# Kernel tuning notes

Measured on AMD Instinct MI355X. Metric: run time of the kernel, lower is better.

Reference implementation:

```python
import jax, jax.numpy as jnp
import numpy as np

D_MODEL = 768; HEADS = 8; LAYERS = 2

def pos_encoding(n, d):
    pos = np.arange(n, dtype=np.float32)[:, None]
    div = np.exp(np.arange(0, d, 2, dtype=np.float32) * -(np.log(10000.0) / d))
    pe = np.zeros((n, d), np.float32)
    pe[:, 0::2] = np.sin(pos * div)
    pe[:, 1::2] = np.cos(pos * div)
    return jnp.asarray(pe)

def layer_norm(x, g, b):
    m = x.mean(-1, keepdims=True)
    v = ((x - m) ** 2).mean(-1, keepdims=True)
    return (x - m) / jnp.sqrt(v + 1e-6) * g + b

def mha(k_in, v_in, q_in, mask, Wq, bq, Wk, bk, Wv, bv, Wout, bout):
    # BertSum MultiHeadedAttention(key, value, query, mask); mask True = blocked
    B, Lq, d = q_in.shape
    dk = d // HEADS
    def proj(x, W, b):
        y = x @ W + b
        return y.reshape(B, x.shape[1], HEADS, dk).transpose(0, 2, 1, 3)
    q = proj(q_in, Wq, bq)
    k = proj(k_in, Wk, bk)
    v = proj(v_in, Wv, bv)
    scores = jnp.einsum('bhqd,bhkd->bhqk', q, k) / jnp.sqrt(jnp.float32(dk))
    scores = jnp.where(mask[:, None, :, :], jnp.float32(-1e18), scores)
    attn = jax.nn.softmax(scores, axis=-1)
    out = jnp.einsum('bhqk,bhkd->bhqd', attn, v).transpose(0, 2, 1, 3).reshape(B, Lq, d)
    return out @ Wout + bout

def ffn(x, W1, b1, W2, b2, g, b):
    # PositionwiseFeedForward: x + w2(gelu(w1(LN(x))))
    return x + jax.nn.gelu(layer_norm(x, g, b) @ W1 + b1) @ W2 + b2

def setup_inputs():
    key = jax.random.key(0)
    ks = jax.random.split(key, 20)
    B, N_TOP, N_OUT, D, DFF, DH = 8, 512, 64, D_MODEL, 3072, 512
    s = 0.02
    return {
        'top_vecs': jax.random.normal(ks[0], (B, N_TOP, D), jnp.float32),
        'inputs': jax.random.normal(ks[1], (B, N_OUT, D), jnp.float32),
        'mask': jnp.ones((B, N_TOP), bool),
        'label_mask': jnp.ones((B, N_OUT), bool),
        'Wq': jax.random.normal(ks[2], (LAYERS, D, D)) * s,
        'bq': jnp.zeros((LAYERS, D)),
        'Wk': jax.random.normal(ks[3], (LAYERS, D, D)) * s,
        'bk': jnp.zeros((LAYERS, D)),
        'Wv': jax.random.normal(ks[4], (LAYERS, D, D)) * s,
        'bv': jnp.zeros((LAYERS, D)),
        'Wout': jax.random.normal(ks[5], (LAYERS, D, D)) * s,
        'bout': jnp.zeros((LAYERS, D)),
        'W1': jax.random.normal(ks[6], (LAYERS, D, DFF)) * s,
        'b1': jnp.zeros((LAYERS, DFF)),
        'W2': jax.random.normal(ks[7], (LAYERS, DFF, D)) * s,
        'b2': jnp.zeros((LAYERS, D)),
        'ln_g': jnp.ones((LAYERS, D)),
        'ln_b': jnp.zeros((LAYERS, D)),
        'Wo': jax.random.normal(ks[8], (D, DH)) * s,
        'bo': jnp.zeros((DH,)),
        'Wi': jax.random.normal(ks[9], (D, DH)) * s,
        'bi': jnp.zeros((DH,)),
        'v_w': jax.random.normal(ks[10], (DH,)) * s,
        'v_b': jnp.zeros(()),
    }

def reference(top_vecs, inputs, mask, label_mask, Wq, bq, Wk, bk, Wv, bv, Wout, bout,
              W1, b1, W2, b2, ln_g, ln_b, Wo, bo, Wi, bi, v_w, v_b):
    B, n_out, d = inputs.shape
    pe = pos_encoding(n_out, d)
    seq_mask = jnp.triu(jnp.ones((n_out, n_out), bool), 1)  # future positions blocked
    self_mask = (~label_mask)[:, None, :] | seq_mask[None]  # (B, n_out, n_out)
    ctx_mask = jnp.broadcast_to((~mask)[:, None, :], (B, n_out, mask.shape[1]))
    x = inputs + pe[None]
    for i in range(LAYERS):
        ctx = mha(x, x, x, self_mask, Wq[i], bq[i], Wk[i], bk[i], Wv[i], bv[i], Wout[i], bout[i])
        dec = mha(top_vecs, top_vecs, ctx, ctx_mask, Wq[i], bq[i], Wk[i], bk[i], Wv[i], bv[i], Wout[i], bout[i])
        x = ffn(dec, W1[i], b1[i], W2[i], b2[i], ln_g[i], ln_b[i])
    # additive-attention scoring head: (B, n_out, n_top, d_hidden) broadcast intermediate
    h = jax.nn.leaky_relu((x @ Wo + bo)[:, :, None, :] + (top_vecs @ Wi + bi)[:, None, :, :])
    scores = jnp.einsum('bonh,h->bon', h, v_w) + v_b
    return jax.nn.softmax(scores, axis=-1)
```

## Files before the change

### kernel.cpp

```cpp
#include <hip/hip_runtime.h>
#include <math.h>

#define D_MODEL 768
#define HEADS   8
#define DK      96
#define NB      8
#define N_TOP   512
#define N_OUT   64
#define DFF     3072
#define DH      512

typedef short  short8  __attribute__((ext_vector_type(8)));
typedef short  short4v __attribute__((ext_vector_type(4)));
typedef float  floatx4 __attribute__((ext_vector_type(4)));

__device__ __forceinline__ unsigned short f2bf(float f) {
    unsigned int u = __float_as_uint(f);
    u += 0x7fffu + ((u >> 16) & 1u);
    return (unsigned short)(u >> 16);
}
__device__ __forceinline__ float bf2f(unsigned short h) {
    return __uint_as_float(((unsigned int)h) << 16);
}

__device__ __forceinline__ float gelu_f(float x) {
    const float c = 0.7978845608028654f;
    return 0.5f * x * (1.0f + tanhf(c * (x + 0.044715f * x * x * x)));
}

__device__ __forceinline__ void gl16(const short* g, short* l) {
    __builtin_amdgcn_global_load_lds(
        (const __attribute__((address_space(1))) void*)g,
        (__attribute__((address_space(3))) void*)l, 16, 0, 0);
}

__device__ __forceinline__ float block_reduce_sum(float v, float* red) {
    int tid = threadIdx.x;
    red[tid] = v;
    __syncthreads();
    for (int s = blockDim.x >> 1; s > 0; s >>= 1) {
        if (tid < s) red[tid] += red[tid + s];
        __syncthreads();
    }
    float r = red[0];
    __syncthreads();
    return r;
}
__device__ __forceinline__ float block_reduce_max(float v, float* red) {
    int tid = threadIdx.x;
    red[tid] = v;
    __syncthreads();
    for (int s = blockDim.x >> 1; s > 0; s >>= 1) {
        if (tid < s) red[tid] = fmaxf(red[tid], red[tid + s]);
        __syncthreads();
    }
    float r = red[0];
    __syncthreads();
    return r;
}

struct TPack {
    const float* src[14];
    short*       dst[14];
    int K[14], N[14];
    int tstart[15];
};

__global__ __launch_bounds__(256) void multi_transpose_kernel(TPack pk) {
    __shared__ float t[32][33];
    int tile = blockIdx.x;
    int i = 0;
    while (i < 13 && tile >= pk.tstart[i + 1]) ++i;
    int lt = tile - pk.tstart[i];
    int K = pk.K[i], N = pk.N[i];
    int ntx = N >> 5;
    int bx = lt % ntx, by = lt / ntx;
    const float* in = pk.src[i];
    short* out = pk.dst[i];
    int tx = threadIdx.x & 31, ty = threadIdx.x >> 5;
#pragma unroll
    for (int r = 0; r < 4; ++r)
        t[ty + r * 8][tx] = in[(size_t)(by * 32 + ty + r * 8) * N + bx * 32 + tx];
    __syncthreads();
#pragma unroll
    for (int r = 0; r < 4; ++r)
        out[(size_t)(bx * 32 + ty + r * 8) * K + by * 32 + tx] =
            (short)f2bf(t[tx][ty + r * 8]);
}

__global__ void prep_kernel(const float* __restrict__ top, const float* __restrict__ inp,
                            short* __restrict__ top_bf, short* __restrict__ xb,
                            const short* __restrict__ WTq0, const short* __restrict__ WTq1,
                            const float* __restrict__ bout, const float* __restrict__ bq,
                            float* __restrict__ bqc,
                            int nkv4, int nx4) {
    int i = blockIdx.x * blockDim.x + threadIdx.x;
    if (i < nkv4) {
        float4 v = ((const float4*)top)[i];
        top_bf[i * 4 + 0] = (short)f2bf(v.x);
        top_bf[i * 4 + 1] = (short)f2bf(v.y);
        top_bf[i * 4 + 2] = (short)f2bf(v.z);
        top_bf[i * 4 + 3] = (short)f2bf(v.w);
        return;
    }
    int j = i - nkv4;
    if (j < nx4) {
#pragma unroll
        for (int u = 0; u < 4; ++u) {
            int idx = j * 4 + u;
            int c   = idx % D_MODEL;
            int pos = (idx / D_MODEL) % N_OUT;
            int jj  = c >> 1;
            float ang = (float)pos * expf((float)(2 * jj) * (-logf(10000.0f) / (float)D_MODEL));
            float pe  = (c & 1) ? cosf(ang) : sinf(ang);
            xb[idx] = (short)f2bf(inp[idx] + pe);
        }
        return;
    }
    int g = j - nx4;
    if (g >= 2 * D_MODEL) return;
    int L = g / D_MODEL, n = g % D_MODEL;
    const short* wr = (L == 0 ? WTq0 : WTq1) + (size_t)n * D_MODEL;
    const float* bo_ = bout + (size_t)L * D_MODEL;
    float s = bq[(size_t)L * D_MODEL + n];
    for (int k = 0; k < D_MODEL; k += 8) {
        short8 w = *(const short8*)(wr + k);
#pragma unroll
        for (int u = 0; u < 8; ++u)
            s += bo_[k + u] * bf2f((unsigned short)w[u]);
    }
    bqc[(size_t)L * D_MODEL + n] = s;
}

struct GDesc {
    const short* A;
    const short* Bt;
    int K;
    int nbx;
    short*       dst[3];
    const float* bias[3];
    int cum[4];
    int vtlog[3];
    int nseg;
};
struct GPack {
    GDesc d[5];
    int nd;
    int start[6];
};

__global__ __launch_bounds__(256) void gemm128g_kernel(GPack gp) {
    __shared__ __align__(16) short As[2 * 64 * 32];
    __shared__ __align__(16) short Bs[2 * 128 * 32];

    const int blk = blockIdx.x;
    int di = 0;
    while (di + 1 < gp.nd && blk >= gp.start[di + 1]) ++di;
    const GDesc& D = gp.d[di];
    const int l = blk - gp.start[di];
    const int bm = (l / D.nbx) * 64, bn = (l % D.nbx) * 128;
    const int K = D.K;
    const int nst = K >> 5;

    const int tid  = threadIdx.x;
    const int wave = tid >> 6, lane = tid & 63;
    const int wr = wave >> 1, wc = wave & 1;
    const int lc = lane & 15;
    const int lq = lane >> 4;
    const int lr4 = lq * 4;
    const int ko  = lq * 8;

    const int srA = wave * 16 + (lane >> 2);
    const int srB = wave * 32 + (lane >> 2);
    const int scol = (lane & 3) * 8;
    const int sbA = wave * 512;
    const int sbB = wave * 1024;

    floatx4 acc[2][4];
#pragma unroll
    for (int i = 0; i < 2; ++i)
#pragma unroll
        for (int j = 0; j < 4; ++j) acc[i][j] = (floatx4)0.0f;

    const short* Ab = D.A  + (size_t)(bm + srA) * K + scol;
    const short* Bb = D.Bt + (size_t)(bn + srB) * K + scol;
    const size_t hq = (size_t)16 * K;

#define STG(t, buf) do {                                          \
        gl16(Ab + (size_t)(t) * 32,      As + (buf) * 2048 + sbA);\
        gl16(Bb + (size_t)(t) * 32,      Bs + (buf) * 4096 + sbB);\
        gl16(Bb + (size_t)(t) * 32 + hq, Bs + (buf) * 4096 + sbB + 512);\
    } while (0)

    STG(0, 0);
    __syncthreads();

    int cur = 0;
    for (int t = 0; t < nst; ++t) {
        if (t + 1 < nst) STG(t + 1, cur ^ 1);
        const short* Ar = As + cur * 2048;
        const short* Br = Bs + cur * 4096;
        short8 a[2], b[4];
#pragma unroll
        for (int f = 0; f < 2; ++f)
            a[f] = *(const short8*)&Ar[(wr * 32 + f * 16 + lc) * 32 + ko];
#pragma unroll
        for (int f = 0; f < 4; ++f)
            b[f] = *(const short8*)&Br[(wc * 64 + f * 16 + lc) * 32 + ko];
#pragma unroll
        for (int fr = 0; fr < 2; ++fr)
#pragma unroll
            for (int fc = 0; fc < 4; ++fc)
                acc[fr][fc] = __builtin_amdgcn_mfma_f32_16x16x32_bf16(
                    a[fr], b[fc], acc[fr][fc], 0, 0, 0);
        __syncthreads();
        cur ^= 1;
    }
#undef STG

#pragma unroll
    for (int fc = 0; fc < 4; ++fc) {
        int col = bn + wc * 64 + fc * 16 + lc;
        int s = 0;
        while (s + 1 < D.nseg && col >= D.cum[s + 1]) ++s;
        int cl   = col - D.cum[s];
        int segw = D.cum[s + 1] - D.cum[s];
        const float* bp = D.bias[s];
        short* dst = D.dst[s];
        int vtl = D.vtlog[s];
        float bi = bp ? bp[cl] : 0.0f;
#pragma unroll
        for (int fr = 0; fr < 2; ++fr)
#pragma unroll
            for (int r = 0; r < 4; ++r) {
                int row = bm + wr * 32 + fr * 16 + lr4 + r;
                float x = acc[fr][fc][r] + bi;
                if (vtl) {
                    int seq = 1 << vtl;
                    dst[((size_t)(row >> vtl) * segw + cl) * seq + (row & (seq - 1))] =
                        (short)f2bf(x);
                } else {
                    dst[(size_t)row * segw + cl] = (short)f2bf(x);
                }
            }
    }
}

__global__ __launch_bounds__(256) void gemm_bf16_kernel(
    const short* __restrict__ A, const short* __restrict__ Bt,
    const float* __restrict__ bias0, const float* __restrict__ bias1,
    const float* __restrict__ bias2, const float* __restrict__ residual,
    float* __restrict__ Cf, short* __restrict__ Cb0, short* __restrict__ Cb1,
    short* __restrict__ Cb2, float* __restrict__ part,
    int M, int N, int K, int act, int segw, int vt_seg, int vt_log) {
    __shared__ __align__(16) short As[2 * 2 * 64 * 32];
    __shared__ __align__(16) short Bs[2 * 2 * 64 * 32];

    const int bm = blockIdx.y * 64, bn = blockIdx.x * 64;
    const int nz = gridDim.z, kz = blockIdx.z;
    const int kchunk = K / nz;

    const int tid  = threadIdx.x;
    const int wave = tid >> 6, lane = tid & 63;
    const int wr = wave >> 1, wc = wave & 1;
    const int lc = lane & 15;
    const int lr4 = (lane >> 4) * 4;
    const int ko  = (lane >> 4) * 8;

    const int srow = wave * 16 + (lane >> 2);
    const int scol = (lane & 3) * 8;
    const int sbase = wave * 512;

    const int nst = kchunk >> 6;

    floatx4 acc[2][2];
#pragma unroll
    for (int i = 0; i < 2; ++i)
#pragma unroll
        for (int j = 0; j < 2; ++j) acc[i][j] = (floatx4)0.0f;

    const short* Ab = A  + (size_t)(bm + srow) * K + kz * kchunk + scol;
    const short* Bb = Bt + (size_t)(bn + srow) * K + kz * kchunk + scol;

#define STG64(t, buf) do {                                    \
        const short* _a = Ab + (size_t)(t) * 64;              \
        const short* _b = Bb + (size_t)(t) * 64;              \
        short* _la = As + (buf) * 4096 + sbase;               \
        short* _lb = Bs + (buf) * 4096 + sbase;               \
        gl16(_a,      _la);                                   \
        gl16(_a + 32, _la + 2048);                            \
        gl16(_b,      _lb);                                   \
        gl16(_b + 32, _lb + 2048);                            \
    } while (0)

    STG64(0, 0);
    __syncthreads();

    int cur = 0;
    for (int t = 0; t < nst; ++t) {
        if (t + 1 < nst) STG64(t + 1, cur ^ 1);
#pragma unroll
        for (int sub = 0; sub < 2; ++sub) {
            const short* Ar = As + cur * 4096 + sub * 2048;
            const short* Br = Bs + cur * 4096 + sub * 2048;
            short8 a0 = *(const short8*)&Ar[(wr * 32 + lc) * 32 + ko];
            short8 a1 = *(const short8*)&Ar[(wr * 32 + 16 + lc) * 32 + ko];
            short8 b0 = *(const short8*)&Br[(wc * 32 + lc) * 32 + ko];
            short8 b1 = *(const short8*)&Br[(wc * 32 + 16 + lc) * 32 + ko];
            acc[0][0] = __builtin_amdgcn_mfma_f32_16x16x32_bf16(a0, b0, acc[0][0], 0, 0, 0);
            acc[0][1] = __builtin_amdgcn_mfma_f32_16x16x32_bf16(a0, b1, acc[0][1], 0, 0, 0);
            acc[1][0] = __builtin_amdgcn_mfma_f32_16x16x32_bf16(a1, b0, acc[1][0], 0, 0, 0);
            acc[1][1] = __builtin_amdgcn_mfma_f32_16x16x32_bf16(a1, b1, acc[1][1], 0, 0, 0);
        }
        __syncthreads();
        cur ^= 1;
    }
#undef STG64

    if (nz > 1) {
        float* pt = part + (size_t)kz * M * N;
#pragma unroll
        for (int fr = 0; fr < 2; ++fr)
#pragma unroll
            for (int fc = 0; fc < 2; ++fc) {
                int col = bn + wc * 32 + fc * 16 + lc;
#pragma unroll
                for (int r = 0; r < 4; ++r) {
                    int row = bm + wr * 32 + fr * 16 + lr4 + r;
                    pt[(size_t)row * N + col] = acc[fr][fc][r];
                }
            }
        return;
    }

#pragma unroll
    for (int fr = 0; fr < 2; ++fr) {
#pragma unroll
        for (int fc = 0; fc < 2; ++fc) {
            int col = bn + wc * 32 + fc * 16 + lc;
            int seg = (col >= segw) + (col >= 2 * segw);
            int cl  = col - seg * segw;
            const float* bp = (seg == 0) ? bias0 : ((seg == 1) ? bias1 : bias2);
            short* dst      = (seg == 0) ? Cb0   : ((seg == 1) ? Cb1   : Cb2);
            float bi = bp ? bp[cl] : 0.0f;
#pragma unroll
            for (int r = 0; r < 4; ++r) {
                int row = bm + wr * 32 + fr * 16 + lr4 + r;
                float x = acc[fr][fc][r] + bi;
                if (residual) x += residual[(size_t)row * N + col];
                if (act == 1) x = gelu_f(x);
                if (Cf) Cf[(size_t)row * N + col] = x;
                if (dst) {
                    if (seg == vt_seg) {
                        int sq = 1 << vt_log;
                        dst[((size_t)(row >> vt_log) * segw + cl) * sq + (row & (sq - 1))] =
                            (short)f2bf(x);
                    } else {
                        dst[(size_t)row * segw + cl] = (short)f2bf(x);
                    }
                }
            }
        }
    }
}

__global__ __launch_bounds__(256) void combine_kernel(
    const float* __restrict__ part, int nz, int N, int MN,
    const float* __restrict__ bias, const float* __restrict__ residual,
    float* __restrict__ Cf, short* __restrict__ Cb) {
    int e = (blockIdx.x * 256 + threadIdx.x) * 4;
    float4 s = *(const float4*)(part + e);
    for (int z = 1; z < nz; ++z) {
        float4 p = *(const float4*)(part + (size_t)z * MN + e);
        s.x += p.x; s.y += p.y; s.z += p.z; s.w += p.w;
    }
    int col = e % N;
    float4 b4 = *(const float4*)(bias + col);
    s.x += b4.x; s.y += b4.y; s.z += b4.z; s.w += b4.w;
    if (residual) {
        float4 r4 = *(const float4*)(residual + e);
        s.x += r4.x; s.y += r4.y; s.z += r4.z; s.w += r4.w;
    }
    if (Cf) *(float4*)(Cf + e) = s;
    if (Cb) {
        short4v o;
        o[0] = (short)f2bf(s.x); o[1] = (short)f2bf(s.y);
        o[2] = (short)f2bf(s.z); o[3] = (short)f2bf(s.w);
        *(short4v*)(Cb + e) = o;
    }
}

__global__ __launch_bounds__(256) void combine_ln_kernel(
    const float* __restrict__ part, int nz,
    const float* __restrict__ bias, const float* __restrict__ g,
    const float* __restrict__ bln,
    float* __restrict__ dec, short* __restrict__ lno) {
    __shared__ float red[256];
    const int MN = 512 * D_MODEL;
    int row = blockIdx.x, tid = threadIdx.x;
    float x[3];
    float s = 0.0f;
#pragma unroll
    for (int i = 0; i < 3; ++i) {
        int c = tid + i * 256;
        float v = bias[c];
        for (int z = 0; z < nz; ++z)
            v += part[(size_t)z * MN + (size_t)row * D_MODEL + c];
        x[i] = v; s += v;
        dec[(size_t)row * D_MODEL + c] = v;
    }
    float mean = block_reduce_sum(s, red) * (1.0f / D_MODEL);
    float vs = 0.0f;
#pragma unroll
    for (int i = 0; i < 3; ++i) {
        float d = x[i] - mean;
        vs += d * d;
    }
    float var = block_reduce_sum(vs, red) * (1.0f / D_MODEL);
    float inv = 1.0f / sqrtf(var + 1e-6f);
#pragma unroll
    for (int i = 0; i < 3; ++i) {
        int c = tid + i * 256;
        lno[(size_t)row * D_MODEL + c] = (short)f2bf((x[i] - mean) * inv * g[c] + bln[c]);
    }
}

template<int LK, bool CAUSAL>
__global__ __launch_bounds__(64) void attn_mfma_kernel(
    const short* __restrict__ Q, const short* __restrict__ K,
    const short* __restrict__ VT, short* __restrict__ out) {
    constexpr int NF = LK / 16;
    constexpr int KS = LK / 32;
    __shared__ __align__(16) short P[16][LK + 8];

    int idx = blockIdx.x;
    const int w = idx & 3;  idx >>= 2;
    const int h = idx & 7;  idx >>= 3;
    const int b = idx;
    const int lane = threadIdx.x;
    const int lc = lane & 15;
    const int lq = lane >> 4;
    const int ko = lq * 8;

    short8 qf[3];
    const short* qbase = Q + ((size_t)(b * N_OUT + w * 16 + lc)) * D_MODEL + h * DK;
#pragma unroll
    for (int s = 0; s < 3; ++s) qf[s] = *(const short8*)(qbase + s * 32 + ko);

    floatx4 acc[NF];
#pragma unroll
    for (int f = 0; f < NF; ++f) acc[f] = (floatx4)0.0f;
    const short* kbase = K + ((size_t)(b * LK)) * D_MODEL + h * DK;
#pragma unroll
    for (int f = 0; f < NF; ++f) {
        const short* kr = kbase + (size_t)(f * 16 + lc) * D_MODEL;
#pragma unroll
        for (int s = 0; s < 3; ++s) {
            short8 kf = *(const short8*)(kr + s * 32 + ko);
            acc[f] = __builtin_amdgcn_mfma_f32_16x16x32_bf16(qf[s], kf, acc[f], 0, 0, 0);
        }
    }

    const float scale = 0.10206207261596575f;
    float inv[4];
#pragma unroll
    for (int r = 0; r < 4; ++r) {
        int row = w * 16 + lq * 4 + r;
        float m = -INFINITY;
#pragma unroll
        for (int f = 0; f < NF; ++f) {
            float s = acc[f][r] * scale;
            if (CAUSAL && (f * 16 + lc) > row) s = -INFINITY;
            acc[f][r] = s;
            m = fmaxf(m, s);
        }
#pragma unroll
        for (int d = 1; d < 16; d <<= 1) m = fmaxf(m, __shfl_xor(m, d));
        float sum = 0.0f;
#pragma unroll
        for (int f = 0; f < NF; ++f) {
            float e = expf(acc[f][r] - m);
            acc[f][r] = e;
            sum += e;
        }
#pragma unroll
        for (int d = 1; d < 16; d <<= 1) sum += __shfl_xor(sum, d);
        inv[r] = 1.0f / sum;
    }

#pragma unroll
    for (int f = 0; f < NF; ++f)
#pragma unroll
        for (int r = 0; r < 4; ++r)
            P[lq * 4 + r][f * 16 + lc] = (short)f2bf(acc[f][r] * inv[r]);
    __syncthreads();

    floatx4 oacc[6];
#pragma unroll
    for (int n = 0; n < 6; ++n) oacc[n] = (floatx4)0.0f;
    const short* vbase = VT + ((size_t)b * D_MODEL + h * DK) * LK;
#pragma unroll
    for (int s = 0; s < KS; ++s) {
        short8 pf = *(const short8*)&P[lc][s * 32 + ko];
#pragma unroll
        for (int n = 0; n < 6; ++n) {
            short8 vf = *(const short8*)(vbase + (size_t)(n * 16 + lc) * LK + s * 32 + ko);
            oacc[n] = __builtin_amdgcn_mfma_f32_16x16x32_bf16(pf, vf, oacc[n], 0, 0, 0);
        }
    }

#pragma unroll
    for (int n = 0; n < 6; ++n)
#pragma unroll
        for (int r = 0; r < 4; ++r) {
            int row = b * N_OUT + w * 16 + lq * 4 + r;
            int col = h * DK + n * 16 + lc;
            out[(size_t)row * D_MODEL + col] = (short)f2bf(oacc[n][r]);
        }
}

__global__ __launch_bounds__(256) void attn_cross_kernel(
    const short* __restrict__ Q, const short* __restrict__ K,
    const short* __restrict__ VT, short* __restrict__ out) {
    constexpr int LK = 512, KW = 128, NF = KW / 16, KS = KW / 32;
    __shared__ __align__(16) short P[4][16][KW + 8];
    __shared__ float Of[4][16][96];
    __shared__ float ms[4][16];
    __shared__ float ss[4][16];

    int idx = blockIdx.x;
    const int w = idx & 3;  idx >>= 2;
    const int h = idx & 7;  idx >>= 3;
    const int b = idx;
    const int tid  = threadIdx.x;
    const int ws   = tid >> 6;
    const int lane = tid & 63;
    const int lc = lane & 15;
    const int lq = lane >> 4;
    const int ko = lq * 8;

    short8 qf[3];
    const short* qbase = Q + ((size_t)(b * N_OUT + w * 16 + lc)) * D_MODEL + h * DK;
#pragma unroll
    for (int s = 0; s < 3; ++s) qf[s] = *(const short8*)(qbase + s * 32 + ko);

    floatx4 acc[NF];
#pragma unroll
    for (int f = 0; f < NF; ++f) acc[f] = (floatx4)0.0f;
    const short* kbase = K + ((size_t)(b * LK + ws * KW)) * D_MODEL + h * DK;
#pragma unroll
    for (int f = 0; f < NF; ++f) {
        const short* kr = kbase + (size_t)(f * 16 + lc) * D_MODEL;
#pragma unroll
        for (int s = 0; s < 3; ++s) {
            short8 kf = *(const short8*)(kr + s * 32 + ko);
            acc[f] = __builtin_amdgcn_mfma_f32_16x16x32_bf16(qf[s], kf, acc[f], 0, 0, 0);
        }
    }

    const float scale = 0.10206207261596575f;
#pragma unroll
    for (int r = 0; r < 4; ++r) {
        float m = -INFINITY;
#pragma unroll
        for (int f = 0; f < NF; ++f) {
            float s = acc[f][r] * scale;
            acc[f][r] = s;
            m = fmaxf(m, s);
        }
#pragma unroll
        for (int d = 1; d < 16; d <<= 1) m = fmaxf(m, __shfl_xor(m, d));
        float sum = 0.0f;
#pragma unroll
        for (int f = 0; f < NF; ++f) {
            float e = expf(acc[f][r] - m);
            acc[f][r] = e;
            sum += e;
        }
#pragma unroll
        for (int d = 1; d < 16; d <<= 1) sum += __shfl_xor(sum, d);
        if (lc == 0) {
            ms[ws][lq * 4 + r] = m;
            ss[ws][lq * 4 + r] = sum;
        }
    }

#pragma unroll
    for (int f = 0; f < NF; ++f)
#pragma unroll
        for (int r = 0; r < 4; ++r)
            P[ws][lq * 4 + r][f * 16 + lc] = (short)f2bf(acc[f][r]);
    __syncthreads();

    floatx4 oacc[6];
#pragma unroll
    for (int n = 0; n < 6; ++n) oacc[n] = (floatx4)0.0f;
    const short* vbase = VT + ((size_t)b * D_MODEL + h * DK) * LK + ws * KW;
#pragma unroll
    for (int s = 0; s < KS; ++s) {
        short8 pf = *(const short8*)&P[ws][lc][s * 32 + ko];
#pragma unroll
        for (int n = 0; n < 6; ++n) {
            short8 vf = *(const short8*)(vbase + (size_t)(n * 16 + lc) * LK + s * 32 + ko);
            oacc[n] = __builtin_amdgcn_mfma_f32_16x16x32_bf16(pf, vf, oacc[n], 0, 0, 0);
        }
    }

#pragma unroll
    for (int n = 0; n < 6; ++n)
#pragma unroll
        for (int r = 0; r < 4; ++r)
            Of[ws][lq * 4 + r][n * 16 + lc] = oacc[n][r];
    __syncthreads();

    for (int e = tid; e < 16 * 96; e += 256) {
        int row = e / 96, col = e - row * 96;
        float m0 = ms[0][row], m1 = ms[1][row], m2 = ms[2][row], m3 = ms[3][row];
        float m = fmaxf(fmaxf(m0, m1), fmaxf(m2, m3));
        float f0 = expf(m0 - m), f1 = expf(m1 - m);
        float f2 = expf(m2 - m), f3 = expf(m3 - m);
        float denom = f0 * ss[0][row] + f1 * ss[1][row] +
                      f2 * ss[2][row] + f3 * ss[3][row];
        float val = f0 * Of[0][row][col] + f1 * Of[1][row][col] +
                    f2 * Of[2][row][col] + f3 * Of[3][row][col];
        out[(size_t)(b * N_OUT + w * 16 + row) * D_MODEL + h * DK + col] =
            (short)f2bf(val / denom);
    }
}

__global__ __launch_bounds__(512) void head_kernel(
    const float* __restrict__ part, const float* __restrict__ bo,
    const short* __restrict__ cb,
    const float* __restrict__ v_w, const float* __restrict__ v_b,
    float* __restrict__ out) {
    __shared__ float as[DH];
    __shared__ float vs[DH];
    __shared__ float red[512];

    int b = blockIdx.x >> 6;
    int o = blockIdx.x & 63;
    int tid = threadIdx.x;

    const int MN = 512 * DH;
    int idx = blockIdx.x * DH + tid;
    as[tid] = part[idx] + part[MN + idx] + part[2 * MN + idx] + bo[tid];
    vs[tid] = v_w[tid];
    __syncthreads();

    const short* crow = cb + ((size_t)b * N_TOP + tid) * DH;
    float s0 = 0.0f, s1 = 0.0f, s2 = 0.0f, s3 = 0.0f;
#pragma unroll 2
    for (int hh = 0; hh < DH; hh += 32) {
        short8 c0 = *(const short8*)(crow + hh);
        short8 c1 = *(const short8*)(crow + hh + 8);
        short8 c2 = *(const short8*)(crow + hh + 16);
        short8 c3 = *(const short8*)(crow + hh + 24);
#pragma unroll
        for (int u = 0; u < 8; ++u) {
            float x0 = as[hh + u]      + bf2f((unsigned short)c0[u]);
            float x1 = as[hh + 8 + u]  + bf2f((unsigned short)c1[u]);
            float x2 = as[hh + 16 + u] + bf2f((unsigned short)c2[u]);
            float x3 = as[hh + 24 + u] + bf2f((unsigned short)c3[u]);
            x0 = fmaxf(x0, 0.0f) + 0.01f * fminf(x0, 0.0f);
            x1 = fmaxf(x1, 0.0f) + 0.01f * fminf(x1, 0.0f);
            x2 = fmaxf(x2, 0.0f) + 0.01f * fminf(x2, 0.0f);
            x3 = fmaxf(x3, 0.0f) + 0.01f * fminf(x3, 0.0f);
            s0 = fmaf(vs[hh + u], x0, s0);
            s1 = fmaf(vs[hh + 8 + u], x1, s1);
            s2 = fmaf(vs[hh + 16 + u], x2, s2);
            s3 = fmaf(vs[hh + 24 + u], x3, s3);
        }
    }
    float s = (s0 + s1) + (s2 + s3) + v_b[0];

    float m = block_reduce_max(s, red);
    float e = expf(s - m);
    float sum = block_reduce_sum(e, red);
    out[((size_t)b * N_OUT + o) * N_TOP + tid] = e / sum;
}

extern "C" void kernel_launch(void* const* d_in, const int* in_sizes, int n_in,
                              void* d_out, int out_size, void* d_ws, size_t ws_size,
                              hipStream_t stream) {
    const float* top  = (const float*)d_in[0];
    const float* inp  = (const float*)d_in[1];
    const float* Wq   = (const float*)d_in[4];
    const float* bq   = (const float*)d_in[5];
    const float* Wk   = (const float*)d_in[6];
    const float* bk   = (const float*)d_in[7];
    const float* Wv   = (const float*)d_in[8];
    const float* bv   = (const float*)d_in[9];
    const float* Wout = (const float*)d_in[10];
    const float* bout = (const float*)d_in[11];
    const float* W1   = (const float*)d_in[12];
    const float* b1   = (const float*)d_in[13];
    const float* W2   = (const float*)d_in[14];
    const float* b2   = (const float*)d_in[15];
    const float* ln_g = (const float*)d_in[16];
    const float* ln_b = (const float*)d_in[17];
    const float* Wo   = (const float*)d_in[18];
    const float* bo   = (const float*)d_in[19];
    const float* Wi   = (const float*)d_in[20];
    const float* bi   = (const float*)d_in[21];
    const float* v_w  = (const float*)d_in[22];
    const float* v_b  = (const float*)d_in[23];

    char* p = (char*)d_ws;
    auto alloc = [&](size_t bytes) -> void* {
        void* r = (void*)p;
        p += (bytes + 255) & ~(size_t)255;
        return r;
    };

    const size_t WSQ = 768 * 768;
    short *WT_q[2], *WT_k[2], *WT_v[2], *WT_o[2], *WT_1[2], *WT_2[2];
    for (int L = 0; L < 2; ++L) {
        WT_q[L] = (short*)alloc(WSQ * 2);
        WT_k[L] = (short*)alloc(WSQ * 2);
        WT_v[L] = (short*)alloc(WSQ * 2);
        WT_o[L] = (short*)alloc(WSQ * 2);
        WT_1[L] = (short*)alloc((size_t)768 * DFF * 2);
        WT_2[L] = (short*)alloc((size_t)768 * DFF * 2);
    }
    short* WT_oh = (short*)alloc((size_t)768 * DH * 2);
    short* WT_ih = (short*)alloc((size_t)768 * DH * 2);
    short* WQC[2];
    WQC[0] = (short*)alloc(WSQ * 2);
    WQC[1] = (short*)alloc(WSQ * 2);
    float* BQC = (float*)alloc(2 * D_MODEL * 4);

    const int NX  = NB * N_OUT * D_MODEL;
    const int NKV = NB * N_TOP * D_MODEL;

    short* top_bf = (short*)alloc((size_t)NKV * 2);
    short* X_bf   = (short*)alloc((size_t)NX * 2);
    short* Q_bf   = (short*)alloc((size_t)NX * 2);
    short* K_bf   = (short*)alloc((size_t)NKV * 2);
    short* VT     = (short*)alloc((size_t)NKV * 2);
    short* AO_bf  = (short*)alloc((size_t)NX * 2);
    float* DEC    = (float*)alloc((size_t)NX * 4);
    short* LNO_bf = (short*)alloc((size_t)NX * 2);
    short* MID_bf = (short*)alloc((size_t)NB * N_OUT * DFF * 2);
    short* c_hb   = (short*)alloc((size_t)NB * N_TOP * DH * 2);
    float* PART   = (float*)alloc((size_t)4 * NX * 4);

    TPack pk;
    {
        int i = 0, t = 0;
        auto put = [&](const float* s, short* d, int K, int N) {
            pk.src[i] = s; pk.dst[i] = d; pk.K[i] = K; pk.N[i] = N;
            pk.tstart[i] = t; t += (K / 32) * (N / 32); ++i;
        };
        for (int L = 0; L < 2; ++L) {
            put(Wq + (size_t)L * WSQ, WT_q[L], 768, 768);
            put(Wk + (size_t)L * WSQ, WT_k[L], 768, 768);
            put(Wv + (size_t)L * WSQ, WT_v[L], 768, 768);
            put(Wout + (size_t)L * WSQ, WT_o[L], 768, 768);
            put(W1 + (size_t)L * 768 * DFF, WT_1[L], 768, DFF);
            put(W2 + (size_t)L * DFF * 768, WT_2[L], DFF, 768);
        }
        put(Wo, WT_oh, 768, DH);
        put(Wi, WT_ih, 768, DH);
        pk.tstart[14] = t;
        hipLaunchKernelGGL(multi_transpose_kernel, dim3(t), dim3(256), 0, stream, pk);
    }

    hipLaunchKernelGGL(prep_kernel,
                       dim3((NKV / 4 + NX / 4 + 2 * D_MODEL + 255) / 256), dim3(256),
                       0, stream, top, inp, top_bf, X_bf,
                       WT_q[0], WT_q[1], bout, bq, BQC, NKV / 4, NX / 4);

    const int MQ = NB * N_OUT;
    const int MT = NB * N_TOP;

    auto G = [&](const short* A, const short* Bt,
                 const float* b0, const float* res, float* Cf, short* C0,
                 int M, int N, int K, int act) {
        hipLaunchKernelGGL(gemm_bf16_kernel, dim3(N / 64, M / 64, 1), dim3(256), 0, stream,
                           A, Bt, b0, nullptr, nullptr, res, Cf, C0, nullptr, nullptr,
                           nullptr, M, N, K, act, N, -1, 0);
    };
    auto GS = [&](const short* A, const short* Bt, const float* b0,
                  const float* res, float* Cf, short* C0,
                  int M, int N, int K, int nz) {
        hipLaunchKernelGGL(gemm_bf16_kernel, dim3(N / 64, M / 64, nz), dim3(256), 0, stream,
                           A, Bt, nullptr, nullptr, nullptr, nullptr,
                           nullptr, nullptr, nullptr, nullptr, PART,
                           M, N, K, 0, N, -1, 0);
        hipLaunchKernelGGL(combine_kernel, dim3(M * N / 1024), dim3(256), 0, stream,
                           PART, nz, N, M * N, b0, res, Cf, C0);
    };

    for (int L = 0; L < 2; ++L) {
        const float* _bq = bq + (size_t)L * D_MODEL;
        const float* _bk = bk + (size_t)L * D_MODEL;
        const float* _bv = bv + (size_t)L * D_MODEL;
        const float* _bo = bout + (size_t)L * D_MODEL;
        const float* _b1 = b1 + (size_t)L * DFF;
        const float* _b2 = b2 + (size_t)L * D_MODEL;
        const float* _g  = ln_g + (size_t)L * D_MODEL;
        const float* _b  = ln_b + (size_t)L * D_MODEL;

        {
            GPack gp{};
            int nd = 0, cum = 0;
            auto putd = [&](const short* A, const short* Bt, int K, int N, int M) {
                GDesc& d = gp.d[nd];
                d.A = A; d.Bt = Bt; d.K = K; d.nbx = N / 128;
                gp.start[nd] = cum;
                cum += (M / 64) * d.nbx;
                return nd++;
            };
            {
                int i = putd(top_bf, WT_k[L], D_MODEL, 1536, MT);
                gp.d[i].dst[0] = K_bf; gp.d[i].bias[0] = _bk; gp.d[i].vtlog[0] = 0;
                gp.d[i].dst[1] = VT;   gp.d[i].bias[1] = _bv; gp.d[i].vtlog[1] = 9;
                gp.d[i].cum[0] = 0; gp.d[i].cum[1] = 768; gp.d[i].cum[2] = 1536;
                gp.d[i].nseg = 2;
            }
            {
                int i = putd(X_bf, WT_q[L], D_MODEL, 2304, MQ);
                gp.d[i].dst[0] = Q_bf;   gp.d[i].bias[0] = _bq; gp.d[i].vtlog[0] = 0;
                gp.d[i].dst[1] = LNO_bf; gp.d[i].bias[1] = _bk; gp.d[i].vtlog[1] = 0;
                gp.d[i].dst[2] = MID_bf; gp.d[i].bias[2] = _bv; gp.d[i].vtlog[2] = 6;
                gp.d[i].cum[0] = 0; gp.d[i].cum[1] = 768; gp.d[i].cum[2] = 1536;
                gp.d[i].cum[3] = 2304; gp.d[i].nseg = 3;
            }
            if (L == 0) {
                int i = putd(top_bf, WT_ih, D_MODEL, DH, MT);
                gp.d[i].dst[0] = c_hb; gp.d[i].bias[0] = bi; gp.d[i].vtlog[0] = 0;
                gp.d[i].cum[0] = 0; gp.d[i].cum[1] = DH; gp.d[i].nseg = 1;
                for (int L2 = 0; L2 < 2; ++L2) {
                    int j = putd(WT_q[L2], WT_o[L2], D_MODEL, 768, 768);
                    gp.d[j].dst[0] = WQC[L2]; gp.d[j].bias[0] = nullptr;
                    gp.d[j].vtlog[0] = 0;
                    gp.d[j].cum[0] = 0; gp.d[j].cum[1] = 768; gp.d[j].nseg = 1;
                }
            }
            gp.nd = nd;
            gp.start[nd] = cum;
            hipLaunchKernelGGL(gemm128g_kernel, dim3(cum), dim3(256), 0, stream, gp);
        }

        hipLaunchKernelGGL((attn_mfma_kernel<64, true>), dim3(NB * HEADS * 4), dim3(64),
                           0, stream, Q_bf, LNO_bf, MID_bf, AO_bf);

        GS(AO_bf, WQC[L], BQC + (size_t)L * D_MODEL, nullptr, nullptr, Q_bf,
           MQ, D_MODEL, D_MODEL, 3);

        hipLaunchKernelGGL(attn_cross_kernel, dim3(NB * HEADS * 4), dim3(256),
                           0, stream, Q_bf, K_bf, VT, AO_bf);
        hipLaunchKernelGGL(gemm_bf16_kernel, dim3(D_MODEL / 64, MQ / 64, 3), dim3(256),
                           0, stream, AO_bf, WT_o[L],
                           nullptr, nullptr, nullptr, nullptr,
                           nullptr, nullptr, nullptr, nullptr, PART,
                           MQ, D_MODEL, D_MODEL, 0, D_MODEL, -1, 0);
        hipLaunchKernelGGL(combine_ln_kernel, dim3(MQ), dim3(256), 0, stream,
                           PART, 3, _bo, _g, _b, DEC, LNO_bf);

        G(LNO_bf, WT_1[L], _b1, nullptr, nullptr, MID_bf, MQ, DFF, D_MODEL, 1);
        GS(MID_bf, WT_2[L], _b2, DEC, nullptr, X_bf, MQ, D_MODEL, DFF, 4);
    }

    hipLaunchKernelGGL(gemm_bf16_kernel, dim3(DH / 64, MQ / 64, 3), dim3(256), 0, stream,
                       X_bf, WT_oh, nullptr, nullptr, nullptr, nullptr,
                       nullptr, nullptr, nullptr, nullptr, PART,
                       MQ, DH, D_MODEL, 0, DH, -1, 0);
    hipLaunchKernelGGL(head_kernel, dim3(NB * N_OUT), dim3(512), 0, stream,
                       PART, bo, c_hb, v_w, v_b, (float*)d_out);
}
```

Before: 444.6 us.

## Hoist both layers' K/V projections into one 128x128 grouped GEMM; fuse Q combine

Enlarges the grouped GEMM tile from 64x128 to 128x128 and launches one grouped GEMM up front that computes K/V for both layers, the head's top-vector projection, the layer-0 QKV, and the folded Wq·Wo weights. K/V buffers are duplicated per layer. Layer 1's QKV projection now uses the regular GEMM kernel. The split-K partials of the folded Q projection are summed with bias inside the cross-attention kernel, which drops a separate combine launch and a bf16 round-trip. The cost is more LDS and register use per block, fewer blocks for the small grouped GEMMs, and extra memory for the second set of K/V buffers.

```diff
diff --git a/kernel.cpp b/kernel.cpp
--- a/kernel.cpp
+++ b/kernel.cpp
@@ -144,13 +144,13 @@
     int nseg;
 };
 struct GPack {
-    GDesc d[5];
+    GDesc d[6];
     int nd;
-    int start[6];
+    int start[7];
 };
 
 __global__ __launch_bounds__(256) void gemm128g_kernel(GPack gp) {
-    __shared__ __align__(16) short As[2 * 64 * 32];
+    __shared__ __align__(16) short As[2 * 128 * 32];
     __shared__ __align__(16) short Bs[2 * 128 * 32];
 
     const int blk = blockIdx.x;
@@ -158,7 +158,7 @@
     while (di + 1 < gp.nd && blk >= gp.start[di + 1]) ++di;
     const GDesc& D = gp.d[di];
     const int l = blk - gp.start[di];
-    const int bm = (l / D.nbx) * 64, bn = (l % D.nbx) * 128;
+    const int bm = (l / D.nbx) * 128, bn = (l % D.nbx) * 128;
     const int K = D.K;
     const int nst = K >> 5;
 
@@ -170,45 +170,47 @@
     const int lr4 = lq * 4;
     const int ko  = lq * 8;
 
-    const int srA = wave * 16 + (lane >> 2);
-    const int srB = wave * 32 + (lane >> 2);
+    const int srow = wave * 32 + (lane >> 2);
     const int scol = (lane & 3) * 8;
-    const int sbA = wave * 512;
-    const int sbB = wave * 1024;
-
-    floatx4 acc[2][4];
-#pragma unroll
-    for (int i = 0; i < 2; ++i)
+    const int sbase = wave * 1024;
+
+    floatx4 acc[4][4];
+#pragma unroll
+    for (int i = 0; i < 4; ++i)
 #pragma unroll
         for (int j = 0; j < 4; ++j) acc[i][j] = (floatx4)0.0f;
 
-    const short* Ab = D.A  + (size_t)(bm + srA) * K + scol;
-    const short* Bb = D.Bt + (size_t)(bn + srB) * K + scol;
+    const short* Ab = D.A  + (size_t)(bm + srow) * K + scol;
+    const short* Bb = D.Bt + (size_t)(bn + srow) * K + scol;
     const size_t hq = (size_t)16 * K;
 
-#define STG(t, buf) do {                                          \
-        gl16(Ab + (size_t)(t) * 32,      As + (buf) * 2048 + sbA);\
-        gl16(Bb + (size_t)(t) * 32,      Bs + (buf) * 4096 + sbB);\
-        gl16(Bb + (size_t)(t) * 32 + hq, Bs + (buf) * 4096 + sbB + 512);\
+#define STG128(t, buf) do {                                   \
+        const short* _a = Ab + (size_t)(t) * 32;              \
+        const short* _b = Bb + (size_t)(t) * 32;              \
+        short* _la = As + (buf) * 4096 + sbase;               \
+        short* _lb = Bs + (buf) * 4096 + sbase;               \
+        gl16(_a,      _la);                                   \
+        gl16(_a + hq, _la + 512);                             \
+        gl16(_b,      _lb);                                   \
+        gl16(_b + hq, _lb + 512);                             \
     } while (0)
 
-    STG(0, 0);
+    STG128(0, 0);
     __syncthreads();
 
     int cur = 0;
     for (int t = 0; t < nst; ++t) {
-        if (t + 1 < nst) STG(t + 1, cur ^ 1);
-        const short* Ar = As + cur * 2048;
+        if (t + 1 < nst) STG128(t + 1, cur ^ 1);
+        const short* Ar = As + cur * 4096;
         const short* Br = Bs + cur * 4096;
-        short8 a[2], b[4];
-#pragma unroll
-        for (int f = 0; f < 2; ++f)
-            a[f] = *(const short8*)&Ar[(wr * 32 + f * 16 + lc) * 32 + ko];
-#pragma unroll
-        for (int f = 0; f < 4; ++f)
+        short8 a[4], b[4];
+#pragma unroll
+        for (int f = 0; f < 4; ++f) {
+            a[f] = *(const short8*)&Ar[(wr * 64 + f * 16 + lc) * 32 + ko];
             b[f] = *(const short8*)&Br[(wc * 64 + f * 16 + lc) * 32 + ko];
-#pragma unroll
-        for (int fr = 0; fr < 2; ++fr)
+        }
+#pragma unroll
+        for (int fr = 0; fr < 4; ++fr)
 #pragma unroll
             for (int fc = 0; fc < 4; ++fc)
                 acc[fr][fc] = __builtin_amdgcn_mfma_f32_16x16x32_bf16(
@@ -216,7 +218,7 @@
         __syncthreads();
         cur ^= 1;
     }
-#undef STG
+#undef STG128
 
 #pragma unroll
     for (int fc = 0; fc < 4; ++fc) {
@@ -230,10 +232,10 @@
         int vtl = D.vtlog[s];
         float bi = bp ? bp[cl] : 0.0f;
 #pragma unroll
-        for (int fr = 0; fr < 2; ++fr)
+        for (int fr = 0; fr < 4; ++fr)
 #pragma unroll
             for (int r = 0; r < 4; ++r) {
-                int row = bm + wr * 32 + fr * 16 + lr4 + r;
+                int row = bm + wr * 64 + fr * 16 + lr4 + r;
                 float x = acc[fr][fc][r] + bi;
                 if (vtl) {
                     int seq = 1 << vtl;
@@ -520,8 +522,9 @@
 }
 
 __global__ __launch_bounds__(256) void attn_cross_kernel(
-    const short* __restrict__ Q, const short* __restrict__ K,
-    const short* __restrict__ VT, short* __restrict__ out) {
+    const float* __restrict__ Qp, const float* __restrict__ bqc,
+    const short* __restrict__ K, const short* __restrict__ VT,
+    short* __restrict__ out) {
     constexpr int LK = 512, KW = 128, NF = KW / 16, KS = KW / 32;
     __shared__ __align__(16) short P[4][16][KW + 8];
     __shared__ float Of[4][16][96];
@@ -539,10 +542,24 @@
     const int lq = lane >> 4;
     const int ko = lq * 8;
 
+    const int MNq = 512 * D_MODEL;
+    const size_t qrow = (size_t)(b * N_OUT + w * 16 + lc) * D_MODEL;
     short8 qf[3];
-    const short* qbase = Q + ((size_t)(b * N_OUT + w * 16 + lc)) * D_MODEL + h * DK;
-#pragma unroll
-    for (int s = 0; s < 3; ++s) qf[s] = *(const short8*)(qbase + s * 32 + ko);
+#pragma unroll
+    for (int s = 0; s < 3; ++s) {
+        int cb = h * DK + s * 32 + ko;
+#pragma unroll
+        for (int v4 = 0; v4 < 2; ++v4) {
+            float4 p0 = *(const float4*)(Qp + qrow + cb + v4 * 4);
+            float4 p1 = *(const float4*)(Qp + (size_t)MNq + qrow + cb + v4 * 4);
+            float4 p2 = *(const float4*)(Qp + (size_t)2 * MNq + qrow + cb + v4 * 4);
+            float4 bb = *(const float4*)(bqc + cb + v4 * 4);
+            qf[s][v4 * 4 + 0] = (short)f2bf(p0.x + p1.x + p2.x + bb.x);
+            qf[s][v4 * 4 + 1] = (short)f2bf(p0.y + p1.y + p2.y + bb.y);
+            qf[s][v4 * 4 + 2] = (short)f2bf(p0.z + p1.z + p2.z + bb.z);
+            qf[s][v4 * 4 + 3] = (short)f2bf(p0.w + p1.w + p2.w + bb.w);
+        }
+    }
 
     floatx4 acc[NF];
 #pragma unroll
@@ -735,8 +752,11 @@
     short* top_bf = (short*)alloc((size_t)NKV * 2);
     short* X_bf   = (short*)alloc((size_t)NX * 2);
     short* Q_bf   = (short*)alloc((size_t)NX * 2);
-    short* K_bf   = (short*)alloc((size_t)NKV * 2);
-    short* VT     = (short*)alloc((size_t)NKV * 2);
+    short* K_bf[2]; short* VT[2];
+    K_bf[0] = (short*)alloc((size_t)NKV * 2);
+    K_bf[1] = (short*)alloc((size_t)NKV * 2);
+    VT[0]   = (short*)alloc((size_t)NKV * 2);
+    VT[1]   = (short*)alloc((size_t)NKV * 2);
     short* AO_bf  = (short*)alloc((size_t)NX * 2);
     float* DEC    = (float*)alloc((size_t)NX * 4);
     short* LNO_bf = (short*)alloc((size_t)NX * 2);
@@ -773,23 +793,47 @@
     const int MQ = NB * N_OUT;
     const int MT = NB * N_TOP;
 
-    auto G = [&](const short* A, const short* Bt,
-                 const float* b0, const float* res, float* Cf, short* C0,
-                 int M, int N, int K, int act) {
-        hipLaunchKernelGGL(gemm_bf16_kernel, dim3(N / 64, M / 64, 1), dim3(256), 0, stream,
-                           A, Bt, b0, nullptr, nullptr, res, Cf, C0, nullptr, nullptr,
-                           nullptr, M, N, K, act, N, -1, 0);
-    };
-    auto GS = [&](const short* A, const short* Bt, const float* b0,
-                  const float* res, float* Cf, short* C0,
-                  int M, int N, int K, int nz) {
-        hipLaunchKernelGGL(gemm_bf16_kernel, dim3(N / 64, M / 64, nz), dim3(256), 0, stream,
-                           A, Bt, nullptr, nullptr, nullptr, nullptr,
-                           nullptr, nullptr, nullptr, nullptr, PART,
-                           M, N, K, 0, N, -1, 0);
-        hipLaunchKernelGGL(combine_kernel, dim3(M * N / 1024), dim3(256), 0, stream,
-                           PART, nz, N, M * N, b0, res, Cf, C0);
-    };
+    {
+        GPack gp{};
+        int nd = 0, cum = 0;
+        auto putd = [&](const short* A, const short* Bt, int K, int N, int M) {
+            GDesc& d = gp.d[nd];
+            d.A = A; d.Bt = Bt; d.K = K; d.nbx = N / 128;
+            gp.start[nd] = cum;
+            cum += (M / 128) * d.nbx;
+            return nd++;
+        };
+        for (int L = 0; L < 2; ++L) {
+            int i = putd(top_bf, WT_k[L], D_MODEL, 1536, MT);
+            gp.d[i].dst[0] = K_bf[L]; gp.d[i].bias[0] = bk + (size_t)L * D_MODEL;
+            gp.d[i].vtlog[0] = 0;
+            gp.d[i].dst[1] = VT[L];   gp.d[i].bias[1] = bv + (size_t)L * D_MODEL;
+            gp.d[i].vtlog[1] = 9;
+            gp.d[i].cum[0] = 0; gp.d[i].cum[1] = 768; gp.d[i].cum[2] = 1536;
+            gp.d[i].nseg = 2;
+        }
+        {
+            int i = putd(top_bf, WT_ih, D_MODEL, DH, MT);
+            gp.d[i].dst[0] = c_hb; gp.d[i].bias[0] = bi; gp.d[i].vtlog[0] = 0;
+            gp.d[i].cum[0] = 0; gp.d[i].cum[1] = DH; gp.d[i].nseg = 1;
+        }
+        {
+            int i = putd(X_bf, WT_q[0], D_MODEL, 2304, MQ);
+            gp.d[i].dst[0] = Q_bf;   gp.d[i].bias[0] = bq; gp.d[i].vtlog[0] = 0;
+            gp.d[i].dst[1] = LNO_bf; gp.d[i].bias[1] = bk; gp.d[i].vtlog[1] = 0;
+            gp.d[i].dst[2] = MID_bf; gp.d[i].bias[2] = bv; gp.d[i].vtlog[2] = 6;
+            gp.d[i].cum[0] = 0; gp.d[i].cum[1] = 768; gp.d[i].cum[2] = 1536;
+            gp.d[i].cum[3] = 2304; gp.d[i].nseg = 3;
+        }
+        for (int L = 0; L < 2; ++L) {
+            int i = putd(WT_q[L], WT_o[L], D_MODEL, 768, 768);
+            gp.d[i].dst[0] = WQC[L]; gp.d[i].bias[0] = nullptr; gp.d[i].vtlog[0] = 0;
+            gp.d[i].cum[0] = 0; gp.d[i].cum[1] = 768; gp.d[i].nseg = 1;
+        }
+        gp.nd = nd;
+        gp.start[nd] = cum;
+        hipLaunchKernelGGL(gemm128g_kernel, dim3(cum), dim3(256), 0, stream, gp);
+    }
 
     for (int L = 0; L < 2; ++L) {
         const float* _bq = bq + (size_t)L * D_MODEL;
@@ -801,55 +845,26 @@
         const float* _g  = ln_g + (size_t)L * D_MODEL;
         const float* _b  = ln_b + (size_t)L * D_MODEL;
 
-        {
-            GPack gp{};
-            int nd = 0, cum = 0;
-            auto putd = [&](const short* A, const short* Bt, int K, int N, int M) {
-                GDesc& d = gp.d[nd];
-                d.A = A; d.Bt = Bt; d.K = K; d.nbx = N / 128;
-                gp.start[nd] = cum;
-                cum += (M / 64) * d.nbx;
-                return nd++;
-            };
-            {
-                int i = putd(top_bf, WT_k[L], D_MODEL, 1536, MT);
-                gp.d[i].dst[0] = K_bf; gp.d[i].bias[0] = _bk; gp.d[i].vtlog[0] = 0;
-                gp.d[i].dst[1] = VT;   gp.d[i].bias[1] = _bv; gp.d[i].vtlog[1] = 9;
-                gp.d[i].cum[0] = 0; gp.d[i].cum[1] = 768; gp.d[i].cum[2] = 1536;
-                gp.d[i].nseg = 2;
-            }
-            {
-                int i = putd(X_bf, WT_q[L], D_MODEL, 2304, MQ);
-                gp.d[i].dst[0] = Q_bf;   gp.d[i].bias[0] = _bq; gp.d[i].vtlog[0] = 0;
-                gp.d[i].dst[1] = LNO_bf; gp.d[i].bias[1] = _bk; gp.d[i].vtlog[1] = 0;
-                gp.d[i].dst[2] = MID_bf; gp.d[i].bias[2] = _bv; gp.d[i].vtlog[2] = 6;
-                gp.d[i].cum[0] = 0; gp.d[i].cum[1] = 768; gp.d[i].cum[2] = 1536;
-                gp.d[i].cum[3] = 2304; gp.d[i].nseg = 3;
-            }
-            if (L == 0) {
-                int i = putd(top_bf, WT_ih, D_MODEL, DH, MT);
-                gp.d[i].dst[0] = c_hb; gp.d[i].bias[0] = bi; gp.d[i].vtlog[0] = 0;
-                gp.d[i].cum[0] = 0; gp.d[i].cum[1] = DH; gp.d[i].nseg = 1;
-                for (int L2 = 0; L2 < 2; ++L2) {
-                    int j = putd(WT_q[L2], WT_o[L2], D_MODEL, 768, 768);
-                    gp.d[j].dst[0] = WQC[L2]; gp.d[j].bias[0] = nullptr;
-                    gp.d[j].vtlog[0] = 0;
-                    gp.d[j].cum[0] = 0; gp.d[j].cum[1] = 768; gp.d[j].nseg = 1;
-                }
-            }
-            gp.nd = nd;
-            gp.start[nd] = cum;
-            hipLaunchKernelGGL(gemm128g_kernel, dim3(cum), dim3(256), 0, stream, gp);
+        if (L == 1) {
+            hipLaunchKernelGGL(gemm_bf16_kernel, dim3(2304 / 64, MQ / 64, 1), dim3(256),
+                               0, stream, X_bf, WT_q[1], _bq, _bk, _bv, nullptr,
+                               nullptr, Q_bf, LNO_bf, MID_bf, nullptr,
+                               MQ, 2304, D_MODEL, 0, 768, 2, 6);
         }
 
         hipLaunchKernelGGL((attn_mfma_kernel<64, true>), dim3(NB * HEADS * 4), dim3(64),
                            0, stream, Q_bf, LNO_bf, MID_bf, AO_bf);
 
-        GS(AO_bf, WQC[L], BQC + (size_t)L * D_MODEL, nullptr, nullptr, Q_bf,
-           MQ, D_MODEL, D_MODEL, 3);
+        hipLaunchKernelGGL(gemm_bf16_kernel, dim3(D_MODEL / 64, MQ / 64, 3), dim3(256),
+                           0, stream, AO_bf, WQC[L],
+                           nullptr, nullptr, nullptr, nullptr,
+                           nullptr, nullptr, nullptr, nullptr, PART,
+                           MQ, D_MODEL, D_MODEL, 0, D_MODEL, -1, 0);
 
         hipLaunchKernelGGL(attn_cross_kernel, dim3(NB * HEADS * 4), dim3(256),
-                           0, stream, Q_bf, K_bf, VT, AO_bf);
+                           0, stream, PART, BQC + (size_t)L * D_MODEL,
+                           K_bf[L], VT[L], AO_bf);
+
         hipLaunchKernelGGL(gemm_bf16_kernel, dim3(D_MODEL / 64, MQ / 64, 3), dim3(256),
                            0, stream, AO_bf, WT_o[L],
                            nullptr, nullptr, nullptr, nullptr,
@@ -858,8 +873,17 @@
         hipLaunchKernelGGL(combine_ln_kernel, dim3(MQ), dim3(256), 0, stream,
                            PART, 3, _bo, _g, _b, DEC, LNO_bf);
 
-        G(LNO_bf, WT_1[L], _b1, nullptr, nullptr, MID_bf, MQ, DFF, D_MODEL, 1);
-        GS(MID_bf, WT_2[L], _b2, DEC, nullptr, X_bf, MQ, D_MODEL, DFF, 4);
+        hipLaunchKernelGGL(gemm_bf16_kernel, dim3(DFF / 64, MQ / 64, 1), dim3(256),
+                           0, stream, LNO_bf, WT_1[L], _b1, nullptr, nullptr, nullptr,
+                           nullptr, MID_bf, nullptr, nullptr, nullptr,
+                           MQ, DFF, D_MODEL, 1, DFF, -1, 0);
+        hipLaunchKernelGGL(gemm_bf16_kernel, dim3(D_MODEL / 64, MQ / 64, 4), dim3(256),
+                           0, stream, MID_bf, WT_2[L],
+                           nullptr, nullptr, nullptr, nullptr,
+                           nullptr, nullptr, nullptr, nullptr, PART,
+                           MQ, D_MODEL, DFF, 0, D_MODEL, -1, 0);
+        hipLaunchKernelGGL(combine_kernel, dim3(MQ * D_MODEL / 1024), dim3(256), 0, stream,
+                           PART, 4, D_MODEL, MQ * D_MODEL, _b2, DEC, nullptr, X_bf);
     }
 
     hipLaunchKernelGGL(gemm_bf16_kernel, dim3(DH / 64, MQ / 64, 3), dim3(256), 0, stream,
```

Measured after the change: 434.1 us (median of 2 runs). 2.3% less time.
